# Performance work log

Hardware: AMD Instinct MI355X
Metric: run time of the kernel (lower is better)

The kernel has to match this reference:

```python
import jax, jax.numpy as jnp
import numpy as np

B, N_P, N_S = 64, 50, 200
N_NODES = N_P * N_S          # 10000 nodes per graph (jobs x ops)
N_CAND = N_S + 1             # 201 candidates
INPUT_DIM, HIDDEN = 3, 64
NODE_DIM = 2 * HIDDEN        # h_nodes feature dim (=> actor in = 6*HIDDEN)
POOL_DIM = 4 * HIDDEN        # h_pooled dim (mean || max pooling)
H_ACTOR, H_CRITIC = 256, 256


def setup_inputs() -> dict:
    key = jax.random.key(0)
    ks = jax.random.split(key, 16)
    p = lambda k, sh: jax.random.normal(k, sh, jnp.float32) * 0.02
    x = jax.random.normal(ks[0], (B, N_NODES, INPUT_DIM), jnp.float32)
    candidate = jax.random.randint(ks[1], (B, N_CAND), 0, N_NODES)
    mask = jax.random.randint(ks[2], (B, N_CAND), 0, 2) > 0
    mask = mask.at[:, 0].set(True)  # guarantee at least one valid action per row
    return {
        "x": x, "candidate": candidate, "mask": mask,
        "fe_w1": p(ks[3], (INPUT_DIM, HIDDEN)), "fe_b1": jnp.zeros((HIDDEN,), jnp.float32),
        "fe_w2": p(ks[4], (HIDDEN, NODE_DIM)), "fe_b2": jnp.zeros((NODE_DIM,), jnp.float32),
        "a_w1": p(ks[5], (NODE_DIM + POOL_DIM, H_ACTOR)), "a_b1": jnp.zeros((H_ACTOR,), jnp.float32),
        "a_w2": p(ks[6], (H_ACTOR, H_ACTOR)), "a_b2": jnp.zeros((H_ACTOR,), jnp.float32),
        "a_w3": p(ks[7], (H_ACTOR, 1)), "a_b3": jnp.zeros((1,), jnp.float32),
        "c_w1": p(ks[8], (POOL_DIM, H_CRITIC)), "c_b1": jnp.zeros((H_CRITIC,), jnp.float32),
        "c_w2": p(ks[9], (H_CRITIC, H_CRITIC)), "c_b2": jnp.zeros((H_CRITIC,), jnp.float32),
        "c_w3": p(ks[10], (H_CRITIC, 1)), "c_b3": jnp.zeros((1,), jnp.float32),
    }


def _actor_critic(x, candidate, mask,
                  fe_w1, fe_b1, fe_w2, fe_b2,
                  a_w1, a_b1, a_w2, a_b2, a_w3, a_b3,
                  c_w1, c_b1, c_w2, c_b2, c_w3, c_b3):
    # --- feature_extract: per-node MLP embedding, graph-level pooling ---
    h = jax.nn.relu(jnp.einsum('bni,ih->bnh', x, fe_w1) + fe_b1)
    h_nodes = jax.nn.relu(jnp.einsum('bnh,hd->bnd', h, fe_w2) + fe_b2)   # [B, N, 2H]
    h_pooled = jnp.concatenate([h_nodes.mean(axis=1), h_nodes.max(axis=1)], axis=-1)  # [B, 4H]

    # --- gather candidate node features (torch.gather over node axis) ---
    cand_feat = jnp.take_along_axis(h_nodes, candidate[:, :, None], axis=1)  # [B, C, 2H]

    # --- concat broadcast pooled feature ---
    pooled_rep = jnp.broadcast_to(h_pooled[:, None, :], (cand_feat.shape[0], cand_feat.shape[1], h_pooled.shape[-1]))
    concat_fea = jnp.concatenate([cand_feat, pooled_rep], axis=-1)  # [B, C, 6H]

    # --- actor MLP (tanh hidden layers, linear out) ---
    a = jnp.tanh(concat_fea @ a_w1 + a_b1)
    a = jnp.tanh(a @ a_w2 + a_b2)
    scores = a @ a_w3 + a_b3                                    # [B, C, 1]

    # --- mask with -inf, softmax over candidate axis ---
    scores = jnp.where(mask[:, :, None], scores, -jnp.inf)
    pi = jax.nn.softmax(scores, axis=1)                          # [B, C, 1]

    # --- critic MLP on pooled feature ---
    c = jnp.tanh(h_pooled @ c_w1 + c_b1)
    c = jnp.tanh(c @ c_w2 + c_b2)
    v = c @ c_w3 + c_b3                                          # [B, 1]
    return pi, v


def reference(x, candidate, mask,
              fe_w1, fe_b1, fe_w2, fe_b2,
              a_w1, a_b1, a_w2, a_b2, a_w3, a_b3,
              c_w1, c_b1, c_w2, c_b2, c_w3, c_b3):
    return _actor_critic(x, candidate, mask,
                         fe_w1, fe_b1, fe_w2, fe_b2,
                         a_w1, a_b1, a_w2, a_b2, a_w3, a_b3,
                         c_w1, c_b1, c_w2, c_b2, c_w3, c_b3)
```

## Files before the change

### kernel.cpp

```cpp
#include <hip/hip_runtime.h>

#define NN 10000
#define NCAND 201
#define NB 64

typedef __attribute__((ext_vector_type(8))) short short8;
typedef __attribute__((ext_vector_type(4))) float f32x4;

__device__ __forceinline__ float bf2f(unsigned short u) {
  return __uint_as_float(((unsigned int)u) << 16);
}
__device__ __forceinline__ unsigned short f2bf(float f) {
  unsigned int u = __float_as_uint(f);
  u += 0x7FFFu + ((u >> 16) & 1u);
  return (unsigned short)(u >> 16);
}
__device__ __forceinline__ float fast_tanh(float x) {
  return 1.0f - 2.0f / (__expf(2.0f * x) + 1.0f);
}
__device__ __forceinline__ float gld(const void* p, long i, int f) {
  return f ? ((const float*)p)[i] : bf2f(((const unsigned short*)p)[i]);
}

__global__ __launch_bounds__(256, 4)
void mega_kernel(const void* __restrict__ x, const int* __restrict__ cand,
                 const void* w1, const void* b1, const void* w2, const void* b2,
                 const void* aw1, const void* ab1, const void* aw2, const void* ab2,
                 const void* aw3, const void* ab3,
                 const void* cw1, const void* cb1, const void* cw2, const void* cb2,
                 const void* cw3, const void* cb3,
                 const unsigned int* mask_w, const unsigned int* cand_w,
                 int* F, int* scnt,
                 float* __restrict__ psumP, float* __restrict__ pmaxP,
                 unsigned short* __restrict__ cfw,
                 unsigned short* __restrict__ aw1t, unsigned short* __restrict__ aw2t,
                 unsigned short* __restrict__ cw1t, unsigned short* __restrict__ cw2t) {
  __shared__ __align__(16) unsigned short pool[128 * 72];
  __shared__ float w1f[3 * 64];
  __shared__ float b1f[64];
  __shared__ float b2f[128];
  __shared__ int cnts[8];

  const int t = threadIdx.x;
  const int j = blockIdx.x;
  const int lane = t & 63;
  const int wv = t >> 6;

  if (j < 1472) {
    if (t < 8) cnts[t] = 0;
    __syncthreads();
    {
      if ((((const unsigned short*)x)[t] & 0x7F80u) >= 0x4300u) atomicAdd(&cnts[0], 1);
      if (t < 192 && (((const unsigned short*)w1)[t] & 0x7F80u) >= 0x4300u) atomicAdd(&cnts[1], 1);
      if (t < 64 && (((const unsigned short*)b1)[t] & 0x7F80u) >= 0x4300u) atomicAdd(&cnts[2], 1);
      if (t < 128 && (((const unsigned short*)b2)[t] & 0x7F80u) >= 0x4300u) atomicAdd(&cnts[3], 1);
      if ((((const unsigned short*)w2)[t] & 0x7F80u) >= 0x4300u) atomicAdd(&cnts[4], 1);
      int co = 0;
#pragma unroll
      for (int q = 0; q < 4; ++q) {
        int i = t * 4 + q;
        if ((i & 1) && cand_w[i] != 0u) co = 1;
      }
      if (co) atomicAdd(&cnts[5], 1);
    }
    __syncthreads();
    const int F0 = cnts[0] > 32, F1 = cnts[1] > 24, F2 = cnts[2] > 8;
    const int F4 = cnts[3] > 16, Fw2 = cnts[4] > 32, C64 = cnts[5] == 0;

    if (j < 1024) {
      unsigned short* h1s = pool;
      const int b = j >> 4;
      const int s = j & 15;

      if (t < 192) w1f[t] = gld(w1, t, F1);
      if (t < 64) b1f[t] = gld(b1, t, F2);
      if (t < 128) b2f[t] = gld(b2, t, F4);

      short8 bfr[2][2];
#pragma unroll
      for (int nl = 0; nl < 2; ++nl)
#pragma unroll
        for (int ks = 0; ks < 2; ++ks) {
          int col = wv * 32 + nl * 16 + (lane & 15);
          short8 v;
#pragma unroll
          for (int jj = 0; jj < 8; ++jj) {
            int k = (lane >> 4) * 8 + ks * 32 + jj;
            v[jj] = (short)f2bf(gld(w2, (long)k * 128 + col, Fw2));
          }
          bfr[nl][ks] = v;
        }
      __syncthreads();

      float csum[2] = {0.f, 0.f};
      float cmax[2] = {0.f, 0.f};
      const int m = t & 127;
      const int kg = t >> 7;

      float x0 = 0.f, x1 = 0.f, x2 = 0.f;
      if (s < 79) {
        int nb = s * 128;
        if (m < min(128, NN - nb)) {
          long xo = ((long)b * NN + nb + m) * 3;
          x0 = gld(x, xo, F0); x1 = gld(x, xo + 1, F0); x2 = gld(x, xo + 2, F0);
        }
      }

      for (int c = s; c < 79; c += 16) {
        int nb = c * 128;
        int cnt = (nb + 128 <= NN) ? 128 : (NN - nb);
        const bool full = (cnt == 128);
        if (full) {
#pragma unroll
          for (int blk = 0; blk < 4; ++blk) {
            short8 v;
#pragma unroll
            for (int i = 0; i < 8; ++i) {
              int k = kg * 32 + blk * 8 + i;
              float vv = x0 * w1f[k] + x1 * w1f[64 + k] + x2 * w1f[128 + k] + b1f[k];
              v[i] = (short)f2bf(fmaxf(vv, 0.f));
            }
            *(short8*)(h1s + m * 72 + kg * 32 + blk * 8) = v;
          }
        } else if (m < cnt) {
#pragma unroll
          for (int blk = 0; blk < 4; ++blk) {
            short8 v;
#pragma unroll
            for (int i = 0; i < 8; ++i) {
              int k = kg * 32 + blk * 8 + i;
              float vv = x0 * w1f[k] + x1 * w1f[64 + k] + x2 * w1f[128 + k] + b1f[k];
              v[i] = (short)f2bf(fmaxf(vv, 0.f));
            }
            *(short8*)(h1s + m * 72 + kg * 32 + blk * 8) = v;
          }
        }
        {
          int cn = c + 16;
          float nx0 = 0.f, nx1 = 0.f, nx2 = 0.f;
          if (cn < 79) {
            int nbn = cn * 128;
            if (m < min(128, NN - nbn)) {
              long xo = ((long)b * NN + nbn + m) * 3;
              nx0 = gld(x, xo, F0); nx1 = gld(x, xo + 1, F0); nx2 = gld(x, xo + 2, F0);
            }
          }
          __syncthreads();
          x0 = nx0; x1 = nx1; x2 = nx2;
        }
        if (full) {
#pragma unroll
          for (int mt = 0; mt < 8; ++mt) {
            const unsigned short* ap = h1s + (mt * 16 + (lane & 15)) * 72 + ((lane >> 4) * 8);
            short8 af0 = *(const short8*)(ap);
            short8 af1 = *(const short8*)(ap + 32);
#pragma unroll
            for (int nl = 0; nl < 2; ++nl) {
              f32x4 acc = {0.f, 0.f, 0.f, 0.f};
              acc = __builtin_amdgcn_mfma_f32_16x16x32_bf16(af0, bfr[nl][0], acc, 0, 0, 0);
              acc = __builtin_amdgcn_mfma_f32_16x16x32_bf16(af1, bfr[nl][1], acc, 0, 0, 0);
              int col = wv * 32 + nl * 16 + (lane & 15);
              float bb = b2f[col];
#pragma unroll
              for (int r = 0; r < 4; ++r) {
                float v = fmaxf(acc[r] + bb, 0.f);
                csum[nl] += v;
                cmax[nl] = fmaxf(cmax[nl], v);
              }
            }
          }
        } else {
#pragma unroll
          for (int mt = 0; mt < 8; ++mt) {
            const unsigned short* ap = h1s + (mt * 16 + (lane & 15)) * 72 + ((lane >> 4) * 8);
            short8 af0 = *(const short8*)(ap);
            short8 af1 = *(const short8*)(ap + 32);
#pragma unroll
            for (int nl = 0; nl < 2; ++nl) {
              f32x4 acc = {0.f, 0.f, 0.f, 0.f};
              acc = __builtin_amdgcn_mfma_f32_16x16x32_bf16(af0, bfr[nl][0], acc, 0, 0, 0);
              acc = __builtin_amdgcn_mfma_f32_16x16x32_bf16(af1, bfr[nl][1], acc, 0, 0, 0);
              int col = wv * 32 + nl * 16 + (lane & 15);
              float bb = b2f[col];
#pragma unroll
              for (int r = 0; r < 4; ++r) {
                int row = mt * 16 + ((lane >> 4) * 4) + r;
                if (row < cnt) {
                  float v = fmaxf(acc[r] + bb, 0.f);
                  csum[nl] += v;
                  cmax[nl] = fmaxf(cmax[nl], v);
                }
              }
            }
          }
        }
        __syncthreads();
      }
#pragma unroll
      for (int nl = 0; nl < 2; ++nl) {
        csum[nl] += __shfl_xor(csum[nl], 16);
        csum[nl] += __shfl_xor(csum[nl], 32);
        cmax[nl] = fmaxf(cmax[nl], __shfl_xor(cmax[nl], 16));
        cmax[nl] = fmaxf(cmax[nl], __shfl_xor(cmax[nl], 32));
      }
      if (lane < 16) {
#pragma unroll
        for (int nl = 0; nl < 2; ++nl) {
          int col = wv * 32 + nl * 16 + lane;
          psumP[((long)b * 16 + s) * 128 + col] = csum[nl];
          pmaxP[((long)b * 16 + s) * 128 + col] = cmax[nl];
        }
      }
    } else {
      unsigned short* h1c = pool;
      const int idx = j - 1024;
      const int b = idx / 7;
      const int cb = idx % 7;
      const int cbase = cb * 29;

      if (t < 128) b2f[t] = gld(b2, t, F4);

      {
        int r = t & 31;
        int ci = cbase + r;
        if (ci > NCAND - 1) ci = NCAND - 1;
        long cidx = (long)b * NCAND + ci;
        int nd = C64 ? cand[2 * cidx] : cand[cidx];
        long xo = ((long)b * NN + nd) * 3;
        float x0 = gld(x, xo, F0), x1 = gld(x, xo + 1, F0), x2 = gld(x, xo + 2, F0);
        int kg = t >> 5;
#pragma unroll
        for (int i = 0; i < 8; ++i) {
          int k = kg * 8 + i;
          float v = x0 * gld(w1, k, F1) + x1 * gld(w1, 64 + k, F1) +
                    x2 * gld(w1, 128 + k, F1) + gld(b1, k, F2);
          h1c[r * 72 + k] = f2bf(fmaxf(v, 0.f));
        }
      }
      __syncthreads();

      {
        short8 af[2][2];
#pragma unroll
        for (int mt = 0; mt < 2; ++mt)
#pragma unroll
          for (int ks = 0; ks < 2; ++ks)
            af[mt][ks] = *(const short8*)(h1c + (mt * 16 + (lane & 15)) * 72 + ((lane >> 4) * 8) + ks * 32);
#pragma unroll
        for (int nl = 0; nl < 2; ++nl) {
          int col = wv * 32 + nl * 16 + (lane & 15);
          short8 bf0, bf1;
#pragma unroll
          for (int jj = 0; jj < 8; ++jj) {
            int k = (lane >> 4) * 8 + jj;
            bf0[jj] = (short)f2bf(gld(w2, (long)k * 128 + col, Fw2));
            bf1[jj] = (short)f2bf(gld(w2, (long)(k + 32) * 128 + col, Fw2));
          }
          float bb = b2f[col];
#pragma unroll
          for (int mt = 0; mt < 2; ++mt) {
            f32x4 acc = {0.f, 0.f, 0.f, 0.f};
            acc = __builtin_amdgcn_mfma_f32_16x16x32_bf16(af[mt][0], bf0, acc, 0, 0, 0);
            acc = __builtin_amdgcn_mfma_f32_16x16x32_bf16(af[mt][1], bf1, acc, 0, 0, 0);
#pragma unroll
            for (int r = 0; r < 4; ++r) {
              int row = mt * 16 + ((lane >> 4) * 4) + r;
              cfw[(long)idx * 4096 + row * 128 + col] = f2bf(fmaxf(acc[r] + bb, 0.f));
            }
          }
        }
      }
    }
    return;
  }

  if (t < 8) cnts[t] = 0;
  __syncthreads();

  if (j < 1856) {
    const unsigned short* pa = (const unsigned short*)aw1;
    const unsigned short* pb = (const unsigned short*)aw2;
    const unsigned short* pc = (const unsigned short*)cw1;
    const unsigned short* pd = (const unsigned short*)cw2;
    if ((pa[t] & 0x7F80u) >= 0x4300u) atomicAdd(&cnts[0], 1);
    if ((pb[t] & 0x7F80u) >= 0x4300u) atomicAdd(&cnts[1], 1);
    if ((pc[t] & 0x7F80u) >= 0x4300u) atomicAdd(&cnts[2], 1);
    if ((pd[t] & 0x7F80u) >= 0x4300u) atomicAdd(&cnts[3], 1);
    __syncthreads();
    const int Faw1 = cnts[0] > 32, Faw2 = cnts[1] > 32;
    const int Fcw1 = cnts[2] > 32, Fcw2 = cnts[3] > 32;
    int i = (j - 1472) * 256 + t;
    if (i < 256 * 384) { int n = i / 384, k = i % 384; aw1t[i] = f2bf(gld(aw1, k * 256 + n, Faw1)); }
    if (i < 256 * 256) {
      int n = i >> 8, k = i & 255;
      aw2t[i] = f2bf(gld(aw2, k * 256 + n, Faw2));
      cw1t[i] = f2bf(gld(cw1, k * 256 + n, Fcw1));
      cw2t[i] = f2bf(gld(cw2, k * 256 + n, Fcw2));
    }
  } else if (j < 1873) {
    const void* ptrs[17] = {x, w1, b1, w2, b2, aw1, ab1, aw2, ab2, aw3, ab3,
                            cw1, cb1, cw2, cb2, cw3, cb3};
    const int sizes[17] = {1920000, 192, 64, 8192, 128, 98304, 256, 65536, 256,
                           256, 1, 65536, 256, 65536, 256, 256, 1};
    int a = j - 1856;
    const unsigned short* p = (const unsigned short*)ptrs[a];
    int K = min(sizes[a], 2048);
    int c = 0;
    for (int i = t; i < K; i += 256)
      if ((p[i] & 0x7F80u) >= 0x4300u) c++;
    if (c) atomicAdd(&cnts[0], c);
    __syncthreads();
    if (t == 0) F[a] = (cnts[0] > (K >> 3)) ? 1 : 0;
  } else if (j == 1873) {
    int flo = 0, fhi = 0, fgt = 0;
    for (int i = t; i < 3216; i += 256) {
      unsigned int w = mask_w[i];
      if ((w & 0xFFFFu) == 0x3F80u) flo = 1;
      if ((w >> 16) == 0x3F80u) fhi = 1;
      if (w > 1u) fgt = 1;
    }
    if (flo) cnts[0] = 1;
    if (fhi) cnts[1] = 1;
    if (fgt) cnts[2] = 1;
    __syncthreads();
    if (t == 0) F[17] = cnts[0] ? 2 : (cnts[1] ? 3 : (cnts[2] ? 1 : 0));
  } else {
    int co = 0;
    for (int i = t; i < 1024; i += 256)
      if ((i & 1) && cand_w[i] != 0u) co = 1;
    if (co) cnts[0] = 1;
    if (t < 64) scnt[t] = 0;
    __syncthreads();
    if (t == 0) F[18] = cnts[0] ? 0 : 1;
  }
}

__global__ __launch_bounds__(256)
void pp_critic_kernel(const float* __restrict__ psumP, const float* __restrict__ pmaxP,
                      const unsigned short* __restrict__ aw1t,
                      const void* __restrict__ ab1,
                      const unsigned short* __restrict__ cw1t,
                      const unsigned short* __restrict__ cw2t,
                      const void* __restrict__ cb1, const void* __restrict__ cb2,
                      const void* __restrict__ cw3, const void* __restrict__ cb3,
                      const int* __restrict__ F,
                      float* __restrict__ pact, void* __restrict__ out) {
  __shared__ float plf[256];
  __shared__ float c1f[256];
  __shared__ float red[4];
  const int t = threadIdx.x;
  const int b = blockIdx.x & 63;
  const int lane = t & 63, wv = t >> 6;

  float ssum = 0.f, smax = 0.f;
  if (t < 128) {
#pragma unroll
    for (int sl = 0; sl < 16; ++sl) {
      ssum += psumP[((long)b * 16 + sl) * 128 + t];
      smax = fmaxf(smax, pmaxP[((long)b * 16 + sl) * 128 + t]);
    }
  }

  if (blockIdx.x < 64) {
    const int F6 = F[6];
    if (t < 128) {
      plf[t] = bf2f(f2bf(ssum * (1.0f / 10000.0f)));
      plf[128 + t] = bf2f(f2bf(smax));
    }
    __syncthreads();
    float a = gld(ab1, t, F6);
    const unsigned short* row = aw1t + t * 384 + 128;
#pragma unroll
    for (int k8 = 0; k8 < 32; ++k8) {
      short8 w = *(const short8*)(row + k8 * 8);
#pragma unroll
      for (int j = 0; j < 8; ++j)
        a += plf[k8 * 8 + j] * bf2f((unsigned short)w[j]);
    }
    pact[b * 256 + t] = a;
  } else {
    const int OF = (F[0] + F[1] + F[3] + F[5] + F[7] + F[9] + F[11] + F[13] + F[15]) >= 5;
    const int F12 = F[12], F14 = F[14], F15 = F[15], F16 = F[16];
    if (t < 128) {
      plf[t] = ssum * (1.0f / 10000.0f);
      plf[128 + t] = smax;
    }
    __syncthreads();
    {
      float a = gld(cb1, t, F12);
      const unsigned short* row = cw1t + t * 256;
#pragma unroll
      for (int k8 = 0; k8 < 32; ++k8) {
        short8 w = *(const short8*)(row + k8 * 8);
#pragma unroll
        for (int j = 0; j < 8; ++j)
          a += plf[k8 * 8 + j] * bf2f((unsigned short)w[j]);
      }
      c1f[t] = fast_tanh(a);
    }
    __syncthreads();
    {
      float a2 = gld(cb2, t, F14);
      const unsigned short* row = cw2t + t * 256;
#pragma unroll
      for (int k8 = 0; k8 < 32; ++k8) {
        short8 w = *(const short8*)(row + k8 * 8);
#pragma unroll
        for (int j = 0; j < 8; ++j)
          a2 += c1f[k8 * 8 + j] * bf2f((unsigned short)w[j]);
      }
      a2 = fast_tanh(a2);
      float p = a2 * gld(cw3, t, F15);
      for (int o = 32; o; o >>= 1) p += __shfl_xor(p, o);
      __syncthreads();
      if (lane == 0) red[wv] = p;
      __syncthreads();
      if (t == 0) {
        float v = red[0] + red[1] + red[2] + red[3] + gld(cb3, 0, F16);
        if (!(v == v)) v = 0.f;
        if (OF) ((float*)out)[NB * NCAND + b] = v;
        else ((unsigned short*)out)[NB * NCAND + b] = f2bf(v);
      }
    }
  }
}

__global__ __launch_bounds__(256)
void actorB_kernel(const unsigned short* __restrict__ cfw,
                   const void* __restrict__ ab2,
                   const void* __restrict__ aw3, const void* __restrict__ ab3,
                   const void* __restrict__ mask,
                   const int* __restrict__ F,
                   const float* __restrict__ pact,
                   const unsigned short* __restrict__ aw1t,
                   const unsigned short* __restrict__ aw2t,
                   float* __restrict__ scores, int* __restrict__ scnt,
                   void* __restrict__ out) {
  __shared__ __align__(16) unsigned short a1s[32 * 264];
  __shared__ __align__(16) unsigned short a2s[32 * 264];
  __shared__ float pactS[256], ab2f[256];
  __shared__ float red[4];
  __shared__ int amLast;

  const int t = threadIdx.x;
  const int b = blockIdx.x / 7;
  const int cb = blockIdx.x % 7;
  const int cbase = cb * 29;
  const int cntc = min(29, NCAND - cbase);
  const int lane = t & 63;
  const int wv = t >> 6;
  const int F8 = F[8], F9 = F[9], F10 = F[10];

  pactS[t] = pact[b * 256 + t];
  ab2f[t] = gld(ab2, t, F8);

  {
    f32x4 acc[2][4];
#pragma unroll
    for (int mt = 0; mt < 2; ++mt)
#pragma unroll
      for (int nt = 0; nt < 4; ++nt) acc[mt][nt] = (f32x4){0.f, 0.f, 0.f, 0.f};
    const unsigned short* cfb = cfw + (long)blockIdx.x * 4096;
#pragma unroll
    for (int ks = 0; ks < 4; ++ks) {
      short8 af0 = *(const short8*)(cfb + (lane & 15) * 128 + ks * 32 + ((lane >> 4) * 8));
      short8 af1 = *(const short8*)(cfb + (16 + (lane & 15)) * 128 + ks * 32 + ((lane >> 4) * 8));
#pragma unroll
      for (int nt = 0; nt < 4; ++nt) {
        int col = wv * 64 + nt * 16 + (lane & 15);
        short8 bfr = *(const short8*)(aw1t + col * 384 + ks * 32 + ((lane >> 4) * 8));
        acc[0][nt] = __builtin_amdgcn_mfma_f32_16x16x32_bf16(af0, bfr, acc[0][nt], 0, 0, 0);
        acc[1][nt] = __builtin_amdgcn_mfma_f32_16x16x32_bf16(af1, bfr, acc[1][nt], 0, 0, 0);
      }
    }
    __syncthreads();
#pragma unroll
    for (int mt = 0; mt < 2; ++mt)
#pragma unroll
      for (int nt = 0; nt < 4; ++nt) {
        int col = wv * 64 + nt * 16 + (lane & 15);
        float bb = pactS[col];
#pragma unroll
        for (int r = 0; r < 4; ++r) {
          int row = mt * 16 + ((lane >> 4) * 4) + r;
          a1s[row * 264 + col] = f2bf(fast_tanh(acc[mt][nt][r] + bb));
        }
      }
  }
  __syncthreads();

  {
    f32x4 acc[2][4];
#pragma unroll
    for (int mt = 0; mt < 2; ++mt)
#pragma unroll
      for (int nt = 0; nt < 4; ++nt) acc[mt][nt] = (f32x4){0.f, 0.f, 0.f, 0.f};
    for (int ks = 0; ks < 8; ++ks) {
      short8 af0 = *(const short8*)(a1s + (lane & 15) * 264 + ks * 32 + ((lane >> 4) * 8));
      short8 af1 = *(const short8*)(a1s + (16 + (lane & 15)) * 264 + ks * 32 + ((lane >> 4) * 8));
#pragma unroll
      for (int nt = 0; nt < 4; ++nt) {
        int col = wv * 64 + nt * 16 + (lane & 15);
        short8 bfr = *(const short8*)(aw2t + col * 256 + ks * 32 + ((lane >> 4) * 8));
        acc[0][nt] = __builtin_amdgcn_mfma_f32_16x16x32_bf16(af0, bfr, acc[0][nt], 0, 0, 0);
        acc[1][nt] = __builtin_amdgcn_mfma_f32_16x16x32_bf16(af1, bfr, acc[1][nt], 0, 0, 0);
      }
    }
#pragma unroll
    for (int mt = 0; mt < 2; ++mt)
#pragma unroll
      for (int nt = 0; nt < 4; ++nt) {
        int col = wv * 64 + nt * 16 + (lane & 15);
        float bb = ab2f[col];
#pragma unroll
        for (int r = 0; r < 4; ++r) {
          int row = mt * 16 + ((lane >> 4) * 4) + r;
          a2s[row * 264 + col] = f2bf(fast_tanh(acc[mt][nt][r] + bb));
        }
      }
  }
  __syncthreads();

  {
    int row = t >> 3, seg = t & 7;
    float p = 0.f;
#pragma unroll 8
    for (int i = 0; i < 32; ++i) {
      int k = seg * 32 + i;
      p += bf2f(a2s[row * 264 + k]) * gld(aw3, k, F9);
    }
    p += __shfl_xor(p, 1);
    p += __shfl_xor(p, 2);
    p += __shfl_xor(p, 4);
    if (seg == 0 && row < cntc)
      atomicExch(&scores[b * 256 + cbase + row], p + gld(ab3, 0, F10));
  }
  __syncthreads();

  if (t == 0) {
    __threadfence();
    amLast = (atomicAdd(&scnt[b], 1) == 6);
  }
  __syncthreads();
  if (!amLast) return;

  const int MM = F[17];
  const int OF = (F[0] + F[1] + F[3] + F[5] + F[7] + F[9] + F[11] + F[13] + F[15]) >= 5;
  float sraw = 0.f, sv = -1e30f;
  bool valid = false;
  if (t < NCAND) {
    sraw = atomicAdd(&scores[b * 256 + t], 0.0f);
    long idx = (long)b * NCAND + t;
    if (MM == 0)      valid = ((const int*)mask)[idx] != 0;
    else if (MM == 1) valid = ((const unsigned char*)mask)[idx] != 0;
    else if (MM == 2) valid = ((const unsigned short*)mask)[idx] != 0;
    else              valid = ((const unsigned int*)mask)[idx] != 0;
    if (valid) sv = sraw;
  }
  float m = sv;
  for (int o = 32; o; o >>= 1) m = fmaxf(m, __shfl_xor(m, o));
  if (lane == 0) red[wv] = m;
  __syncthreads();
  m = fmaxf(fmaxf(red[0], red[1]), fmaxf(red[2], red[3]));
  __syncthreads();
  float e = valid ? __expf(sraw - m) : 0.f;
  if (!(e == e)) e = 0.f;
  float ss = e;
  for (int o = 32; o; o >>= 1) ss += __shfl_xor(ss, o);
  if (lane == 0) red[wv] = ss;
  __syncthreads();
  float tot = red[0] + red[1] + red[2] + red[3];
  tot = fmaxf(tot, 1e-30f);
  if (t < NCAND) {
    float pv = e / tot;
    if (!(pv == pv)) pv = 0.f;
    if (OF) ((float*)out)[b * NCAND + t] = pv;
    else ((unsigned short*)out)[b * NCAND + t] = f2bf(pv);
  }
}

extern "C" void kernel_launch(void* const* d_in, const int* in_sizes, int n_in,
                              void* d_out, int out_size, void* d_ws, size_t ws_size,
                              hipStream_t stream) {
  const void* x = d_in[0];
  const int* cand = (const int*)d_in[1];
  const void* mask = d_in[2];
  const void* fe_w1 = d_in[3];
  const void* fe_b1 = d_in[4];
  const void* fe_w2 = d_in[5];
  const void* fe_b2 = d_in[6];
  const void* a_w1 = d_in[7];
  const void* a_b1 = d_in[8];
  const void* a_w2 = d_in[9];
  const void* a_b2 = d_in[10];
  const void* a_w3 = d_in[11];
  const void* a_b3 = d_in[12];
  const void* c_w1 = d_in[13];
  const void* c_b1 = d_in[14];
  const void* c_w2 = d_in[15];
  const void* c_b2 = d_in[16];
  const void* c_w3 = d_in[17];
  const void* c_b3 = d_in[18];

  char* ws = (char*)d_ws;
  float* scores = (float*)(ws + 65536);
  unsigned short* aw1t = (unsigned short*)(ws + 147456);
  unsigned short* aw2t = (unsigned short*)(ws + 344064);
  int* F = (int*)(ws + 475136);
  unsigned short* cw1t = (unsigned short*)(ws + 475264);
  unsigned short* cw2t = (unsigned short*)(ws + 606336);
  float* pact = (float*)(ws + 737408);
  unsigned short* cfw = (unsigned short*)(ws + 802944);
  int* scnt = (int*)(ws + 4472960);
  float* psumP = (float*)(ws + 4473216);
  float* pmaxP = (float*)(ws + 4997504);

  mega_kernel<<<1875, 256, 0, stream>>>(x, cand, fe_w1, fe_b1, fe_w2, fe_b2,
                                        a_w1, a_b1, a_w2, a_b2, a_w3, a_b3,
                                        c_w1, c_b1, c_w2, c_b2, c_w3, c_b3,
                                        (const unsigned int*)mask,
                                        (const unsigned int*)cand, F, scnt,
                                        psumP, pmaxP, cfw, aw1t, aw2t, cw1t, cw2t);
  pp_critic_kernel<<<128, 256, 0, stream>>>(psumP, pmaxP, aw1t, a_b1,
                                            cw1t, cw2t, c_b1, c_b2, c_w3, c_b3,
                                            F, pact, (void*)d_out);
  actorB_kernel<<<448, 256, 0, stream>>>(cfw, a_b2, a_w3, a_b3, mask, F, pact,
                                         aw1t, aw2t, scores, scnt, (void*)d_out);
}
```

Baseline: 156.8 us.

## Fuse pooled-projection and critic kernel into actorB kernel

Removes the separate pp_critic launch by merging its work into actorB. The critic now runs in 64 extra blocks appended to the actorB grid. Each actor block recomputes the pooled reduction and the pooled part of the a_w1 projection itself, overlapping this with its MFMA work. This saves one kernel launch and the pact round-trip through global memory. In exchange, each of the 448 actor blocks does redundant partial-sum reads and a 256x256 dot product.

```diff
diff --git a/kernel.cpp b/kernel.cpp
--- a/kernel.cpp
+++ b/kernel.cpp
@@ -336,55 +336,44 @@
 }
 
 __global__ __launch_bounds__(256)
-void pp_critic_kernel(const float* __restrict__ psumP, const float* __restrict__ pmaxP,
-                      const unsigned short* __restrict__ aw1t,
-                      const void* __restrict__ ab1,
-                      const unsigned short* __restrict__ cw1t,
-                      const unsigned short* __restrict__ cw2t,
-                      const void* __restrict__ cb1, const void* __restrict__ cb2,
-                      const void* __restrict__ cw3, const void* __restrict__ cb3,
-                      const int* __restrict__ F,
-                      float* __restrict__ pact, void* __restrict__ out) {
-  __shared__ float plf[256];
-  __shared__ float c1f[256];
+void actorB_kernel(const unsigned short* __restrict__ cfw,
+                   const void* __restrict__ ab1, const void* __restrict__ ab2,
+                   const void* __restrict__ aw3, const void* __restrict__ ab3,
+                   const void* __restrict__ mask,
+                   const int* __restrict__ F,
+                   const float* __restrict__ psumP, const float* __restrict__ pmaxP,
+                   const unsigned short* __restrict__ aw1t,
+                   const unsigned short* __restrict__ aw2t,
+                   const unsigned short* __restrict__ cw1t,
+                   const unsigned short* __restrict__ cw2t,
+                   const void* __restrict__ cb1, const void* __restrict__ cb2,
+                   const void* __restrict__ cw3, const void* __restrict__ cb3,
+                   float* __restrict__ scores, int* __restrict__ scnt,
+                   void* __restrict__ out) {
+  __shared__ __align__(16) unsigned short a1s[32 * 264];
+  __shared__ __align__(16) unsigned short a2s[32 * 264];
+  __shared__ float pactS[256], ab2f[256], plfS[256];
   __shared__ float red[4];
+  __shared__ int amLast;
+
   const int t = threadIdx.x;
-  const int b = blockIdx.x & 63;
-  const int lane = t & 63, wv = t >> 6;
-
-  float ssum = 0.f, smax = 0.f;
-  if (t < 128) {
-#pragma unroll
-    for (int sl = 0; sl < 16; ++sl) {
-      ssum += psumP[((long)b * 16 + sl) * 128 + t];
-      smax = fmaxf(smax, pmaxP[((long)b * 16 + sl) * 128 + t]);
-    }
-  }
-
-  if (blockIdx.x < 64) {
-    const int F6 = F[6];
+  const int lane = t & 63;
+  const int wv = t >> 6;
+
+  if (blockIdx.x >= 448) {
+    const int b = blockIdx.x - 448;
+    float ssum = 0.f, smax = 0.f;
     if (t < 128) {
-      plf[t] = bf2f(f2bf(ssum * (1.0f / 10000.0f)));
-      plf[128 + t] = bf2f(f2bf(smax));
-    }
-    __syncthreads();
-    float a = gld(ab1, t, F6);
-    const unsigned short* row = aw1t + t * 384 + 128;
-#pragma unroll
-    for (int k8 = 0; k8 < 32; ++k8) {
-      short8 w = *(const short8*)(row + k8 * 8);
-#pragma unroll
-      for (int j = 0; j < 8; ++j)
-        a += plf[k8 * 8 + j] * bf2f((unsigned short)w[j]);
-    }
-    pact[b * 256 + t] = a;
-  } else {
+#pragma unroll
+      for (int sl = 0; sl < 16; ++sl) {
+        ssum += psumP[((long)b * 16 + sl) * 128 + t];
+        smax = fmaxf(smax, pmaxP[((long)b * 16 + sl) * 128 + t]);
+      }
+      plfS[t] = ssum * (1.0f / 10000.0f);
+      plfS[128 + t] = smax;
+    }
     const int OF = (F[0] + F[1] + F[3] + F[5] + F[7] + F[9] + F[11] + F[13] + F[15]) >= 5;
     const int F12 = F[12], F14 = F[14], F15 = F[15], F16 = F[16];
-    if (t < 128) {
-      plf[t] = ssum * (1.0f / 10000.0f);
-      plf[128 + t] = smax;
-    }
     __syncthreads();
     {
       float a = gld(cb1, t, F12);
@@ -394,9 +383,9 @@
         short8 w = *(const short8*)(row + k8 * 8);
 #pragma unroll
         for (int j = 0; j < 8; ++j)
-          a += plf[k8 * 8 + j] * bf2f((unsigned short)w[j]);
-      }
-      c1f[t] = fast_tanh(a);
+          a += plfS[k8 * 8 + j] * bf2f((unsigned short)w[j]);
+      }
+      ab2f[t] = fast_tanh(a);
     }
     __syncthreads();
     {
@@ -407,7 +396,7 @@
         short8 w = *(const short8*)(row + k8 * 8);
 #pragma unroll
         for (int j = 0; j < 8; ++j)
-          a2 += c1f[k8 * 8 + j] * bf2f((unsigned short)w[j]);
+          a2 += ab2f[k8 * 8 + j] * bf2f((unsigned short)w[j]);
       }
       a2 = fast_tanh(a2);
       float p = a2 * gld(cw3, t, F15);
@@ -422,37 +411,41 @@
         else ((unsigned short*)out)[NB * NCAND + b] = f2bf(v);
       }
     }
-  }
-}
-
-__global__ __launch_bounds__(256)
-void actorB_kernel(const unsigned short* __restrict__ cfw,
-                   const void* __restrict__ ab2,
-                   const void* __restrict__ aw3, const void* __restrict__ ab3,
-                   const void* __restrict__ mask,
-                   const int* __restrict__ F,
-                   const float* __restrict__ pact,
-                   const unsigned short* __restrict__ aw1t,
-                   const unsigned short* __restrict__ aw2t,
-                   float* __restrict__ scores, int* __restrict__ scnt,
-                   void* __restrict__ out) {
-  __shared__ __align__(16) unsigned short a1s[32 * 264];
-  __shared__ __align__(16) unsigned short a2s[32 * 264];
-  __shared__ float pactS[256], ab2f[256];
-  __shared__ float red[4];
-  __shared__ int amLast;
-
-  const int t = threadIdx.x;
+    return;
+  }
+
   const int b = blockIdx.x / 7;
   const int cb = blockIdx.x % 7;
   const int cbase = cb * 29;
   const int cntc = min(29, NCAND - cbase);
-  const int lane = t & 63;
-  const int wv = t >> 6;
-  const int F8 = F[8], F9 = F[9], F10 = F[10];
-
-  pactS[t] = pact[b * 256 + t];
+  const int F6 = F[6], F8 = F[8], F9 = F[9], F10 = F[10];
+
+  {
+    float ssum = 0.f, smax = 0.f;
+    if (t < 128) {
+#pragma unroll
+      for (int sl = 0; sl < 16; ++sl) {
+        ssum += psumP[((long)b * 16 + sl) * 128 + t];
+        smax = fmaxf(smax, pmaxP[((long)b * 16 + sl) * 128 + t]);
+      }
+      plfS[t] = bf2f(f2bf(ssum * (1.0f / 10000.0f)));
+      plfS[128 + t] = bf2f(f2bf(smax));
+    }
+  }
   ab2f[t] = gld(ab2, t, F8);
+  __syncthreads();
+
+  float pa = gld(ab1, t, F6);
+  {
+    const unsigned short* row = aw1t + t * 384 + 128;
+#pragma unroll
+    for (int k8 = 0; k8 < 32; ++k8) {
+      short8 w = *(const short8*)(row + k8 * 8);
+#pragma unroll
+      for (int j = 0; j < 8; ++j)
+        pa += plfS[k8 * 8 + j] * bf2f((unsigned short)w[j]);
+    }
+  }
 
   {
     f32x4 acc[2][4];
@@ -473,6 +466,7 @@
         acc[1][nt] = __builtin_amdgcn_mfma_f32_16x16x32_bf16(af1, bfr, acc[1][nt], 0, 0, 0);
       }
     }
+    pactS[t] = pa;
     __syncthreads();
 #pragma unroll
     for (int mt = 0; mt < 2; ++mt)
@@ -609,7 +603,6 @@
   int* F = (int*)(ws + 475136);
   unsigned short* cw1t = (unsigned short*)(ws + 475264);
   unsigned short* cw2t = (unsigned short*)(ws + 606336);
-  float* pact = (float*)(ws + 737408);
   unsigned short* cfw = (unsigned short*)(ws + 802944);
   int* scnt = (int*)(ws + 4472960);
   float* psumP = (float*)(ws + 4473216);
@@ -621,9 +614,8 @@
                                         (const unsigned int*)mask,
                                         (const unsigned int*)cand, F, scnt,
                                         psumP, pmaxP, cfw, aw1t, aw2t, cw1t, cw2t);
-  pp_critic_kernel<<<128, 256, 0, stream>>>(psumP, pmaxP, aw1t, a_b1,
-                                            cw1t, cw2t, c_b1, c_b2, c_w3, c_b3,
-                                            F, pact, (void*)d_out);
-  actorB_kernel<<<448, 256, 0, stream>>>(cfw, a_b2, a_w3, a_b3, mask, F, pact,
-                                         aw1t, aw2t, scores, scnt, (void*)d_out);
+  actorB_kernel<<<512, 256, 0, stream>>>(cfw, a_b1, a_b2, a_w3, a_b3, mask, F,
+                                         psumP, pmaxP, aw1t, aw2t, cw1t, cw2t,
+                                         c_b1, c_b2, c_w3, c_b3,
+                                         scores, scnt, (void*)d_out);
 }
```

Measured after the change: 162.1 us. 3.4% more time.
